# Optimization experiments

Measured on AMD Instinct MI355X. Metric: run time of the kernel, lower is better.

## Reference

```python
import jax, jax.numpy as jnp
import numpy as np

BIAS = 0.0001
TEMPERATURE = 1.0


def setup_inputs() -> dict:
    key = jax.random.key(0)
    k_h, k_w1, k_w2, k_u = jax.random.split(key, 4)
    N, H, Z = 8192, 64, 128
    h = jax.random.normal(k_h, (N, H), dtype=jnp.float32)
    W1 = jax.random.normal(k_w1, (H, H), dtype=jnp.float32) * (1.0 / np.sqrt(H))
    b1 = jnp.zeros((H,), dtype=jnp.float32)
    W2 = jax.random.normal(k_w2, (H, Z), dtype=jnp.float32) * (1.0 / np.sqrt(H))
    b2 = jnp.zeros((Z,), dtype=jnp.float32)
    noise_u = jax.random.uniform(k_u, (N, N), dtype=jnp.float32)
    return {"h": h, "W1": W1, "b1": b1, "W2": W2, "b2": b2, "noise_u": noise_u}


def reference(h, W1, b1, W2, b2, noise_u):
    # MLPA: Linear -> ReLU -> Linear, then outer-product adjacency logits
    Zmat = jnp.maximum(h @ W1 + b1, 0.0) @ W2 + b2          # [N, dim_z]
    adj_logits = Zmat @ Zmat.T                               # [N, N]
    # gumbel-sigmoid edge sampling (training path)
    eps = (2.0 * BIAS - 1.0) * noise_u + (1.0 - BIAS)        # uniform in [bias, 1-bias]
    gate = (jnp.log(eps) - jnp.log1p(-eps) + adj_logits) / TEMPERATURE
    adj = jax.nn.sigmoid(gate)
    # keep strict upper triangle, symmetrize
    adj = jnp.triu(adj, 1)
    adj = adj + adj.T
    # fill_diagonal_(1)
    N = adj.shape[0]
    idx = jnp.arange(N)
    adj = adj.at[idx, idx].set(1.0)
    # D^{-1/2} @ adj @ D^{-1/2} expressed as row/col rescale (same math)
    d = jnp.power(adj.sum(axis=1), -0.5)                     # [N]
    adj_norm = d[:, None] * adj * d[None, :]
    return adj_norm, adj_logits
```

## Files before the change

kernel.cpp:

```cpp
#include <hip/hip_runtime.h>
#include <hip/hip_bf16.h>
#include <math.h>

#define N 8192
#define ZD 128
#define NTILE 64
#define NUPPER 2080

typedef __attribute__((ext_vector_type(8))) _Float16 f16x8;
typedef __attribute__((ext_vector_type(4))) float f32x4;

__device__ __forceinline__ int tri_cum(int ti) {
    return (ti * (2 * NTILE + 1 - ti)) / 2;
}

__device__ __forceinline__ void tile_decode(int t, int& ti, int& tj) {
    int est = (int)((129.0f - sqrtf(16641.0f - 8.0f * (float)t)) * 0.5f);
    if (est < 0) est = 0;
    while (tri_cum(est) > t) --est;
    while (tri_cum(est + 1) <= t) ++est;
    ti = est;
    tj = est + (t - tri_cum(est));
}

__global__ __launch_bounds__(256) void k1_mlp(
    const float* __restrict__ h, const float* __restrict__ W1,
    const float* __restrict__ b1, const float* __restrict__ W2,
    const float* __restrict__ b2, _Float16* __restrict__ Zf,
    float* __restrict__ sums)
{
    __shared__ float W1s[64][65];
    __shared__ float W2s[64][129];
    __shared__ float hs[32][68];
    __shared__ float Ts[32][68];
    __shared__ float b1s[64];
    __shared__ float b2s[128];
    const int tid = threadIdx.x;
    const int row0 = blockIdx.x * 32;

    if (tid < 32) sums[row0 + tid] = 1.0f;

    for (int e = tid; e < 64 * 64; e += 256) W1s[e >> 6][e & 63] = W1[e];
    for (int e = tid; e < 64 * 128; e += 256) W2s[e >> 7][e & 127] = W2[e];
    for (int e = tid; e < 32 * 64; e += 256) hs[e >> 6][e & 63] = h[(size_t)row0 * 64 + e];
    if (tid < 64) b1s[tid] = b1[tid];
    if (tid < 128) b2s[tid] = b2[tid];
    __syncthreads();

    {
        const int c = tid & 63;
        const int r0 = (tid >> 6) * 8;
        float s[8];
        #pragma unroll
        for (int j = 0; j < 8; ++j) s[j] = b1s[c];
        #pragma unroll
        for (int k0 = 0; k0 < 64; k0 += 4) {
            const float w0 = W1s[k0 + 0][c], w1 = W1s[k0 + 1][c];
            const float w2 = W1s[k0 + 2][c], w3 = W1s[k0 + 3][c];
            #pragma unroll
            for (int j = 0; j < 8; ++j) {
                f32x4 hv = *(const f32x4*)&hs[r0 + j][k0];
                s[j] = fmaf(hv[0], w0, s[j]);
                s[j] = fmaf(hv[1], w1, s[j]);
                s[j] = fmaf(hv[2], w2, s[j]);
                s[j] = fmaf(hv[3], w3, s[j]);
            }
        }
        #pragma unroll
        for (int j = 0; j < 8; ++j) Ts[r0 + j][c] = fmaxf(s[j], 0.0f);
    }
    __syncthreads();

    {
        const int c = tid & 127;
        const int r0 = (tid >> 7) * 16;
        float s[16];
        #pragma unroll
        for (int j = 0; j < 16; ++j) s[j] = b2s[c];
        #pragma unroll
        for (int k0 = 0; k0 < 64; k0 += 4) {
            const float w0 = W2s[k0 + 0][c], w1 = W2s[k0 + 1][c];
            const float w2 = W2s[k0 + 2][c], w3 = W2s[k0 + 3][c];
            #pragma unroll
            for (int j = 0; j < 16; ++j) {
                f32x4 tv = *(const f32x4*)&Ts[r0 + j][k0];
                s[j] = fmaf(tv[0], w0, s[j]);
                s[j] = fmaf(tv[1], w1, s[j]);
                s[j] = fmaf(tv[2], w2, s[j]);
                s[j] = fmaf(tv[3], w3, s[j]);
            }
        }
        #pragma unroll
        for (int j = 0; j < 16; ++j)
            Zf[(size_t)(row0 + r0 + j) * ZD + c] = (_Float16)s[j];
    }
}

__global__ __launch_bounds__(256, 3) void k3_main(
    const _Float16* __restrict__ Zf, const float* __restrict__ noise,
    float* __restrict__ logits, unsigned char* __restrict__ vws,
    float* __restrict__ sums)
{
    int ti, tj;
    tile_decode(blockIdx.x, ti, tj);
    const bool diag = (ti == tj);

    __shared__ float T[128][65];
    __shared__ float rs[128], cs[128];

    const int tid = threadIdx.x;
    const int lane = tid & 63;
    const int w = tid >> 6;
    const int wr = w >> 1, wc = w & 1;
    const int fr = lane & 15;
    const int kg = lane >> 4;
    const int i0 = ti * 128, j0 = tj * 128;

    unsigned char* __restrict__ vtile = vws + (size_t)blockIdx.x * (128 * 128);

    if (tid < 128) { rs[tid] = 0.0f; cs[tid] = 0.0f; }

    const _Float16* Ap = Zf + (size_t)(i0 + wr * 64) * ZD;
    const _Float16* Bp = Zf + (size_t)(j0 + wc * 64) * ZD;

    f32x4 acc[4][4];
    #pragma unroll
    for (int mf = 0; mf < 4; ++mf)
        #pragma unroll
        for (int nf = 0; nf < 4; ++nf)
            acc[mf][nf] = (f32x4)0.0f;

    #pragma unroll
    for (int kc = 0; kc < 4; ++kc) {
        const int ko = kc * 32 + kg * 8;
        f16x8 a[4], b[4];
        #pragma unroll
        for (int mf = 0; mf < 4; ++mf) {
            size_t off = (size_t)(mf * 16 + fr) * ZD + ko;
            a[mf] = *(const f16x8*)(Ap + off);
            b[mf] = *(const f16x8*)(Bp + off);
        }
        #pragma unroll
        for (int mf = 0; mf < 4; ++mf)
            #pragma unroll
            for (int nf = 0; nf < 4; ++nf)
                acc[mf][nf] = __builtin_amdgcn_mfma_f32_16x16x32_f16(a[mf], b[nf], acc[mf][nf], 0, 0, 0);
    }

    const int c4 = (tid & 15) * 4;
    const int rbase = tid >> 4;

    #pragma unroll
    for (int half = 0; half < 2; ++half) {
        __syncthreads();
        if (wc == half) {
            #pragma unroll
            for (int mf = 0; mf < 4; ++mf)
                #pragma unroll
                for (int nf = 0; nf < 4; ++nf)
                    #pragma unroll
                    for (int r = 0; r < 4; ++r)
                        T[wr * 64 + mf * 16 + (lane >> 4) * 4 + r][nf * 16 + fr] = acc[mf][nf][r];
        }
        __syncthreads();

        f32x4 csum = (f32x4)0.0f;
        #pragma unroll
        for (int it = 0; it < 8; ++it) {
            const int r = rbase + it * 16;
            f32x4 L4 = *(const f32x4*)&T[r][c4];
            const size_t g = (size_t)(i0 + r) * N + j0 + half * 64 + c4;
            __builtin_nontemporal_store(L4, (f32x4*)&logits[g]);
            f32x4 u4 = __builtin_nontemporal_load((const f32x4*)&noise[g]);
            float rsum = 0.0f;
            unsigned q = 0;
            #pragma unroll
            for (int e = 0; e < 4; ++e) {
                float u = u4[e];
                float eps = fmaf(-0.9998f, u, 0.9999f);
                float om  = fmaf( 0.9998f, u, 0.0001f);
                float gate = __logf(eps) - __logf(om) + L4[e];
                float v = 1.0f / (1.0f + __expf(-gate));
                if (diag && r >= half * 64 + c4 + e) v = 0.0f;
                q |= ((unsigned)(int)rintf(v * 255.0f)) << (8 * e);
                rsum += v;
                csum[e] += v;
            }
            __builtin_nontemporal_store(q, (unsigned*)&vtile[r * 128 + half * 64 + c4]);
            atomicAdd(&rs[r], rsum);
        }
        #pragma unroll
        for (int e = 0; e < 4; ++e)
            atomicAdd(&cs[half * 64 + c4 + e], csum[e]);

        if (!diag) {
            #pragma unroll
            for (int it = 0; it < 8; ++it) {
                const int idx = tid + it * 256;
                const int c = idx >> 5;
                const int m4 = (idx & 31) * 4;
                f32x4 o;
                o[0] = T[m4 + 0][c]; o[1] = T[m4 + 1][c];
                o[2] = T[m4 + 2][c]; o[3] = T[m4 + 3][c];
                __builtin_nontemporal_store(o, (f32x4*)&logits[(size_t)(j0 + half * 64 + c) * N + i0 + m4]);
            }
        }
    }

    __syncthreads();
    if (tid < 128) {
        if (diag) {
            atomicAdd(&sums[i0 + tid], rs[tid] + cs[tid]);
        } else {
            atomicAdd(&sums[i0 + tid], rs[tid]);
            atomicAdd(&sums[j0 + tid], cs[tid]);
        }
    }
}

__global__ __launch_bounds__(256, 4) void k5_norm(
    const unsigned char* __restrict__ vws, float* __restrict__ adj,
    const float* __restrict__ sums)
{
    int ti, tj;
    tile_decode(blockIdx.x, ti, tj);
    const bool diag = (ti == tj);
    __shared__ float T[128][68];
    __shared__ float drow[128], dcol[128];
    const int tid = threadIdx.x;
    const int i0 = ti * 128, j0 = tj * 128;

    const unsigned char* __restrict__ vtile = vws + (size_t)blockIdx.x * (128 * 128);

    if (tid < 128) drow[tid] = rsqrtf(sums[i0 + tid]);
    else dcol[tid - 128] = rsqrtf(sums[j0 + tid - 128]);
    __syncthreads();

    const float inv255 = 1.0f / 255.0f;
    #pragma unroll 4
    for (int it = 0; it < 16; ++it) {
        int w = tid + it * 256;
        int m = w >> 5;
        int n4 = (w & 31) << 2;
        unsigned q = __builtin_nontemporal_load((const unsigned*)&vtile[m * 128 + n4]);
        float dm = drow[m];
        f32x4 o;
        o[0] = (float)(q & 255)         * inv255 * dm * dcol[n4 + 0];
        o[1] = (float)((q >> 8) & 255)  * inv255 * dm * dcol[n4 + 1];
        o[2] = (float)((q >> 16) & 255) * inv255 * dm * dcol[n4 + 2];
        o[3] = (float)(q >> 24)         * inv255 * dm * dcol[n4 + 3];
        __builtin_nontemporal_store(o, (f32x4*)&adj[(size_t)(i0 + m) * N + j0 + n4]);
        T[n4 + 0][m] = o[0]; T[n4 + 1][m] = o[1];
        T[n4 + 2][m] = o[2]; T[n4 + 3][m] = o[3];
    }
    __syncthreads();
    #pragma unroll 4
    for (int it = 0; it < 16; ++it) {
        int w = tid + it * 256;
        int c = w >> 5;
        int m4 = (w & 31) << 2;
        f32x4 o = *(const f32x4*)&T[c][m4];
        if (!diag) {
            __builtin_nontemporal_store(o, (f32x4*)&adj[(size_t)(j0 + c) * N + i0 + m4]);
        } else {
            #pragma unroll
            for (int e = 0; e < 4; ++e)
                if (m4 + e < c)
                    adj[(size_t)(j0 + c) * N + i0 + m4 + e] = o[e];
        }
    }
    if (diag && tid < 128) {
        float dm = drow[tid];
        adj[(size_t)(i0 + tid) * N + i0 + tid] = dm * dm;
    }
}

extern "C" void kernel_launch(void* const* d_in, const int* in_sizes, int n_in,
                              void* d_out, int out_size, void* d_ws, size_t ws_size,
                              hipStream_t stream)
{
    const float* h     = (const float*)d_in[0];
    const float* W1    = (const float*)d_in[1];
    const float* b1    = (const float*)d_in[2];
    const float* W2    = (const float*)d_in[3];
    const float* b2    = (const float*)d_in[4];
    const float* noise = (const float*)d_in[5];

    float* adj    = (float*)d_out;
    float* logits = adj + (size_t)N * N;

    _Float16* Zf       = (_Float16*)d_ws;
    unsigned char* vws = (unsigned char*)(Zf + (size_t)N * ZD);
    float* sums        = (float*)(vws + (size_t)NUPPER * 128 * 128);

    k1_mlp<<<256, 256, 0, stream>>>(h, W1, b1, W2, b2, Zf, sums);
    k3_main<<<NUPPER, 256, 0, stream>>>(Zf, noise, logits, vws, sums);
    k5_norm<<<NUPPER, 256, 0, stream>>>(vws, adj, sums);
}
```

Measured before the change: 230.2 us.

## Write full symmetric quantized adjacency in main kernel and stream rows in norm pass

```diff
diff --git a/kernel.cpp b/kernel.cpp
--- a/kernel.cpp
+++ b/kernel.cpp
@@ -9,6 +9,7 @@
 
 typedef __attribute__((ext_vector_type(8))) _Float16 f16x8;
 typedef __attribute__((ext_vector_type(4))) float f32x4;
+typedef __attribute__((ext_vector_type(4))) unsigned int u32x4;
 
 __device__ __forceinline__ int tri_cum(int ti) {
     return (ti * (2 * NTILE + 1 - ti)) / 2;
@@ -70,7 +71,6 @@
         for (int j = 0; j < 8; ++j) Ts[r0 + j][c] = fmaxf(s[j], 0.0f);
     }
     __syncthreads();
-
     {
         const int c = tid & 127;
         const int r0 = (tid >> 7) * 16;
@@ -96,17 +96,24 @@
     }
 }
 
-__global__ __launch_bounds__(256, 3) void k3_main(
+#define AROW 136
+
+__global__ __launch_bounds__(256, 2) void k3_main(
     const _Float16* __restrict__ Zf, const float* __restrict__ noise,
-    float* __restrict__ logits, unsigned char* __restrict__ vws,
+    float* __restrict__ logits, unsigned char* __restrict__ vfull,
     float* __restrict__ sums)
 {
     int ti, tj;
-    tile_decode(blockIdx.x, ti, tj);
+    const int t = (blockIdx.x & 7) * (NUPPER / 8) + (blockIdx.x >> 3);
+    tile_decode(t, ti, tj);
     const bool diag = (ti == tj);
 
-    __shared__ float T[128][65];
+    __shared__ _Float16 smem[2 * 128 * AROW];
     __shared__ float rs[128], cs[128];
+    _Float16* As = smem;
+    _Float16* Bs = smem + 128 * AROW;
+    float (*T)[65] = (float(*)[65])smem;
+    unsigned char* vT = (unsigned char*)(smem + 128 * AROW);
 
     const int tid = threadIdx.x;
     const int lane = tid & 63;
@@ -116,12 +123,15 @@
     const int kg = lane >> 4;
     const int i0 = ti * 128, j0 = tj * 128;
 
-    unsigned char* __restrict__ vtile = vws + (size_t)blockIdx.x * (128 * 128);
-
+    #pragma unroll
+    for (int p = 0; p < 8; ++p) {
+        const int c = tid + p * 256;
+        const int row = c >> 4, cg = (c & 15) << 3;
+        *(f16x8*)&As[row * AROW + cg] = *(const f16x8*)(Zf + (size_t)(i0 + row) * ZD + cg);
+        *(f16x8*)&Bs[row * AROW + cg] = *(const f16x8*)(Zf + (size_t)(j0 + row) * ZD + cg);
+    }
     if (tid < 128) { rs[tid] = 0.0f; cs[tid] = 0.0f; }
-
-    const _Float16* Ap = Zf + (size_t)(i0 + wr * 64) * ZD;
-    const _Float16* Bp = Zf + (size_t)(j0 + wc * 64) * ZD;
+    __syncthreads();
 
     f32x4 acc[4][4];
     #pragma unroll
@@ -136,9 +146,8 @@
         f16x8 a[4], b[4];
         #pragma unroll
         for (int mf = 0; mf < 4; ++mf) {
-            size_t off = (size_t)(mf * 16 + fr) * ZD + ko;
-            a[mf] = *(const f16x8*)(Ap + off);
-            b[mf] = *(const f16x8*)(Bp + off);
+            a[mf] = *(const f16x8*)&As[(wr * 64 + mf * 16 + fr) * AROW + ko];
+            b[mf] = *(const f16x8*)&Bs[(wc * 64 + mf * 16 + fr) * AROW + ko];
         }
         #pragma unroll
         for (int mf = 0; mf < 4; ++mf)
@@ -169,7 +178,8 @@
         for (int it = 0; it < 8; ++it) {
             const int r = rbase + it * 16;
             f32x4 L4 = *(const f32x4*)&T[r][c4];
-            const size_t g = (size_t)(i0 + r) * N + j0 + half * 64 + c4;
+            const int lc0 = half * 64 + c4;
+            const size_t g = (size_t)(i0 + r) * N + j0 + lc0;
             __builtin_nontemporal_store(L4, (f32x4*)&logits[g]);
             f32x4 u4 = __builtin_nontemporal_load((const f32x4*)&noise[g]);
             float rsum = 0.0f;
@@ -181,28 +191,47 @@
                 float om  = fmaf( 0.9998f, u, 0.0001f);
                 float gate = __logf(eps) - __logf(om) + L4[e];
                 float v = 1.0f / (1.0f + __expf(-gate));
-                if (diag && r >= half * 64 + c4 + e) v = 0.0f;
+                if (diag && r >= lc0 + e) v = 0.0f;
                 q |= ((unsigned)(int)rintf(v * 255.0f)) << (8 * e);
                 rsum += v;
                 csum[e] += v;
             }
-            __builtin_nontemporal_store(q, (unsigned*)&vtile[r * 128 + half * 64 + c4]);
+            if (!diag) {
+                __builtin_nontemporal_store(q, (unsigned*)&vfull[g]);
+            } else {
+                #pragma unroll
+                for (int e = 0; e < 4; ++e)
+                    if (r < lc0 + e) vfull[g + e] = (unsigned char)((q >> (8 * e)) & 255);
+            }
+            #pragma unroll
+            for (int e = 0; e < 4; ++e)
+                vT[(c4 + e) * 128 + r] = (unsigned char)((q >> (8 * e)) & 255);
             atomicAdd(&rs[r], rsum);
         }
         #pragma unroll
         for (int e = 0; e < 4; ++e)
             atomicAdd(&cs[half * 64 + c4 + e], csum[e]);
 
-        if (!diag) {
-            #pragma unroll
-            for (int it = 0; it < 8; ++it) {
-                const int idx = tid + it * 256;
-                const int c = idx >> 5;
-                const int m4 = (idx & 31) * 4;
+        __syncthreads();
+
+        #pragma unroll
+        for (int it = 0; it < 8; ++it) {
+            const int idx = tid + it * 256;
+            const int c = idx >> 5;
+            const int m4 = (idx & 31) * 4;
+            const unsigned qd = *(const unsigned*)&vT[c * 128 + m4];
+            if (!diag) {
                 f32x4 o;
                 o[0] = T[m4 + 0][c]; o[1] = T[m4 + 1][c];
                 o[2] = T[m4 + 2][c]; o[3] = T[m4 + 3][c];
                 __builtin_nontemporal_store(o, (f32x4*)&logits[(size_t)(j0 + half * 64 + c) * N + i0 + m4]);
+                __builtin_nontemporal_store(qd, (unsigned*)&vfull[(size_t)(j0 + half * 64 + c) * N + i0 + m4]);
+            } else {
+                const int rr = half * 64 + c;
+                #pragma unroll
+                for (int e = 0; e < 4; ++e)
+                    if (m4 + e < rr)
+                        vfull[(size_t)(i0 + rr) * N + i0 + m4 + e] = (unsigned char)((qd >> (8 * e)) & 255);
             }
         }
     }
@@ -218,60 +247,51 @@
     }
 }
 
-__global__ __launch_bounds__(256, 4) void k5_norm(
-    const unsigned char* __restrict__ vws, float* __restrict__ adj,
-    const float* __restrict__ sums)
-{
-    int ti, tj;
-    tile_decode(blockIdx.x, ti, tj);
-    const bool diag = (ti == tj);
-    __shared__ float T[128][68];
-    __shared__ float drow[128], dcol[128];
+__global__ void k4_dvec(const float* __restrict__ sums, float* __restrict__ dvec)
+{
+    int i = blockIdx.x * 256 + threadIdx.x;
+    if (i < N) dvec[i] = rsqrtf(sums[i]);
+}
+
+__global__ __launch_bounds__(256) void k5_norm(
+    const unsigned char* __restrict__ vfull, float* __restrict__ adj,
+    const float* __restrict__ dvec)
+{
+    __shared__ float dc[N];
     const int tid = threadIdx.x;
-    const int i0 = ti * 128, j0 = tj * 128;
-
-    const unsigned char* __restrict__ vtile = vws + (size_t)blockIdx.x * (128 * 128);
-
-    if (tid < 128) drow[tid] = rsqrtf(sums[i0 + tid]);
-    else dcol[tid - 128] = rsqrtf(sums[j0 + tid - 128]);
-    __syncthreads();
-
-    const float inv255 = 1.0f / 255.0f;
-    #pragma unroll 4
+    #pragma unroll
+    for (int p = 0; p < 8; ++p) {
+        const int e = (tid + p * 256) * 4;
+        *(f32x4*)&dc[e] = *(const f32x4*)&dvec[e];
+    }
+    __syncthreads();
+
+    const int row = blockIdx.x * 8 + (tid >> 5);
+    const float di = dc[row];
+    const float sdi = di * (1.0f / 255.0f);
+    const size_t rowbase = (size_t)row * N;
+    const int lane32 = tid & 31;
+
     for (int it = 0; it < 16; ++it) {
-        int w = tid + it * 256;
-        int m = w >> 5;
-        int n4 = (w & 31) << 2;
-        unsigned q = __builtin_nontemporal_load((const unsigned*)&vtile[m * 128 + n4]);
-        float dm = drow[m];
-        f32x4 o;
-        o[0] = (float)(q & 255)         * inv255 * dm * dcol[n4 + 0];
-        o[1] = (float)((q >> 8) & 255)  * inv255 * dm * dcol[n4 + 1];
-        o[2] = (float)((q >> 16) & 255) * inv255 * dm * dcol[n4 + 2];
-        o[3] = (float)(q >> 24)         * inv255 * dm * dcol[n4 + 3];
-        __builtin_nontemporal_store(o, (f32x4*)&adj[(size_t)(i0 + m) * N + j0 + n4]);
-        T[n4 + 0][m] = o[0]; T[n4 + 1][m] = o[1];
-        T[n4 + 2][m] = o[2]; T[n4 + 3][m] = o[3];
-    }
-    __syncthreads();
-    #pragma unroll 4
-    for (int it = 0; it < 16; ++it) {
-        int w = tid + it * 256;
-        int c = w >> 5;
-        int m4 = (w & 31) << 2;
-        f32x4 o = *(const f32x4*)&T[c][m4];
-        if (!diag) {
-            __builtin_nontemporal_store(o, (f32x4*)&adj[(size_t)(j0 + c) * N + i0 + m4]);
-        } else {
-            #pragma unroll
-            for (int e = 0; e < 4; ++e)
-                if (m4 + e < c)
-                    adj[(size_t)(j0 + c) * N + i0 + m4 + e] = o[e];
-        }
-    }
-    if (diag && tid < 128) {
-        float dm = drow[tid];
-        adj[(size_t)(i0 + tid) * N + i0 + tid] = dm * dm;
+        const int j = (lane32 + it * 32) * 16;
+        u32x4 qv = __builtin_nontemporal_load((const u32x4*)&vfull[rowbase + j]);
+        const bool hasdiag = ((unsigned)(row - j) < 16u);
+        #pragma unroll
+        for (int k = 0; k < 4; ++k) {
+            f32x4 dk = *(const f32x4*)&dc[j + 4 * k];
+            const unsigned qd = qv[k];
+            f32x4 o;
+            o[0] = (float)(qd & 255)         * sdi * dk[0];
+            o[1] = (float)((qd >> 8) & 255)  * sdi * dk[1];
+            o[2] = (float)((qd >> 16) & 255) * sdi * dk[2];
+            o[3] = (float)(qd >> 24)         * sdi * dk[3];
+            if (hasdiag) {
+                #pragma unroll
+                for (int e = 0; e < 4; ++e)
+                    if (j + 4 * k + e == row) o[e] = di * di;
+            }
+            __builtin_nontemporal_store(o, (f32x4*)&adj[rowbase + j + 4 * k]);
+        }
     }
 }
 
@@ -289,11 +309,13 @@
     float* adj    = (float*)d_out;
     float* logits = adj + (size_t)N * N;
 
-    _Float16* Zf       = (_Float16*)d_ws;
-    unsigned char* vws = (unsigned char*)(Zf + (size_t)N * ZD);
-    float* sums        = (float*)(vws + (size_t)NUPPER * 128 * 128);
+    _Float16* Zf         = (_Float16*)d_ws;
+    unsigned char* vfull = (unsigned char*)(Zf + (size_t)N * ZD);
+    float* sums          = (float*)(vfull + (size_t)N * N);
+    float* dvec          = sums + N;
 
     k1_mlp<<<256, 256, 0, stream>>>(h, W1, b1, W2, b2, Zf, sums);
-    k3_main<<<NUPPER, 256, 0, stream>>>(Zf, noise, logits, vws, sums);
-    k5_norm<<<NUPPER, 256, 0, stream>>>(vws, adj, sums);
-}
+    k3_main<<<NUPPER, 256, 0, stream>>>(Zf, noise, logits, vfull, sums);
+    k4_dvec<<<32, 256, 0, stream>>>(sums, dvec);
+    k5_norm<<<N / 8, 256, 0, stream>>>(vfull, adj, dvec);
+}
```

Measured after the change: 686.1 us. 2.98x slower.

## Split k3 tiles into half-width blocks and write results directly from MFMA registers

Applied to the files above, without the earlier changes.

```diff
diff --git a/kernel.cpp b/kernel.cpp
--- a/kernel.cpp
+++ b/kernel.cpp
@@ -70,7 +70,6 @@
         for (int j = 0; j < 8; ++j) Ts[r0 + j][c] = fmaxf(s[j], 0.0f);
     }
     __syncthreads();
-
     {
         const int c = tid & 127;
         const int r0 = (tid >> 7) * 16;
@@ -96,126 +95,114 @@
     }
 }
 
-__global__ __launch_bounds__(256, 3) void k3_main(
+__global__ __launch_bounds__(256, 5) void k3_main(
     const _Float16* __restrict__ Zf, const float* __restrict__ noise,
     float* __restrict__ logits, unsigned char* __restrict__ vws,
     float* __restrict__ sums)
 {
+    const int tt = blockIdx.x >> 1;
+    const int t = (tt & 7) * (NUPPER / 8) + (tt >> 3);
+    const int h = blockIdx.x & 1;
     int ti, tj;
-    tile_decode(blockIdx.x, ti, tj);
+    tile_decode(t, ti, tj);
     const bool diag = (ti == tj);
-
-    __shared__ float T[128][65];
-    __shared__ float rs[128], cs[128];
+    const int i0 = ti * 128;
+    const int j0 = tj * 128 + h * 64;
+
+    __shared__ unsigned char vTT[128 * 68];
+    __shared__ float rs[128], cs[64];
 
     const int tid = threadIdx.x;
     const int lane = tid & 63;
     const int w = tid >> 6;
-    const int wr = w >> 1, wc = w & 1;
+    const int wr = w >> 1, wcc = w & 1;
     const int fr = lane & 15;
     const int kg = lane >> 4;
-    const int i0 = ti * 128, j0 = tj * 128;
-
-    unsigned char* __restrict__ vtile = vws + (size_t)blockIdx.x * (128 * 128);
-
-    if (tid < 128) { rs[tid] = 0.0f; cs[tid] = 0.0f; }
+
+    if (tid < 128) rs[tid] = 0.0f;
+    if (tid < 64) cs[tid] = 0.0f;
 
     const _Float16* Ap = Zf + (size_t)(i0 + wr * 64) * ZD;
-    const _Float16* Bp = Zf + (size_t)(j0 + wc * 64) * ZD;
-
-    f32x4 acc[4][4];
+    const _Float16* Bp = Zf + (size_t)(j0 + wcc * 32) * ZD;
+
+    f32x4 acc[4][2];
     #pragma unroll
     for (int mf = 0; mf < 4; ++mf)
         #pragma unroll
-        for (int nf = 0; nf < 4; ++nf)
+        for (int nf = 0; nf < 2; ++nf)
             acc[mf][nf] = (f32x4)0.0f;
 
     #pragma unroll
     for (int kc = 0; kc < 4; ++kc) {
         const int ko = kc * 32 + kg * 8;
-        f16x8 a[4], b[4];
-        #pragma unroll
-        for (int mf = 0; mf < 4; ++mf) {
-            size_t off = (size_t)(mf * 16 + fr) * ZD + ko;
-            a[mf] = *(const f16x8*)(Ap + off);
-            b[mf] = *(const f16x8*)(Bp + off);
-        }
+        f16x8 a[4], b[2];
         #pragma unroll
         for (int mf = 0; mf < 4; ++mf)
-            #pragma unroll
-            for (int nf = 0; nf < 4; ++nf)
+            a[mf] = *(const f16x8*)(Ap + (size_t)(mf * 16 + fr) * ZD + ko);
+        #pragma unroll
+        for (int nf = 0; nf < 2; ++nf)
+            b[nf] = *(const f16x8*)(Bp + (size_t)(nf * 16 + fr) * ZD + ko);
+        #pragma unroll
+        for (int mf = 0; mf < 4; ++mf)
+            #pragma unroll
+            for (int nf = 0; nf < 2; ++nf)
                 acc[mf][nf] = __builtin_amdgcn_mfma_f32_16x16x32_f16(a[mf], b[nf], acc[mf][nf], 0, 0, 0);
     }
-
-    const int c4 = (tid & 15) * 4;
-    const int rbase = tid >> 4;
-
-    #pragma unroll
-    for (int half = 0; half < 2; ++half) {
-        __syncthreads();
-        if (wc == half) {
-            #pragma unroll
-            for (int mf = 0; mf < 4; ++mf)
-                #pragma unroll
-                for (int nf = 0; nf < 4; ++nf)
-                    #pragma unroll
-                    for (int r = 0; r < 4; ++r)
-                        T[wr * 64 + mf * 16 + (lane >> 4) * 4 + r][nf * 16 + fr] = acc[mf][nf][r];
-        }
-        __syncthreads();
-
-        f32x4 csum = (f32x4)0.0f;
-        #pragma unroll
-        for (int it = 0; it < 8; ++it) {
-            const int r = rbase + it * 16;
-            f32x4 L4 = *(const f32x4*)&T[r][c4];
-            const size_t g = (size_t)(i0 + r) * N + j0 + half * 64 + c4;
-            __builtin_nontemporal_store(L4, (f32x4*)&logits[g]);
-            f32x4 u4 = __builtin_nontemporal_load((const f32x4*)&noise[g]);
-            float rsum = 0.0f;
+    __syncthreads();
+
+    float cacc[2] = {0.f, 0.f};
+    #pragma unroll
+    for (int mf = 0; mf < 4; ++mf) {
+        const int Rl = wr * 64 + mf * 16 + (lane >> 4) * 4;
+        f32x4 rsum4 = (f32x4)0.0f;
+        #pragma unroll
+        for (int nf = 0; nf < 2; ++nf) {
+            const int Cl = wcc * 32 + nf * 16 + (lane & 15);
+            const f32x4 Lv = acc[mf][nf];
+            const size_t gi = (size_t)(i0 + Rl) * N + (j0 + Cl);
+            #pragma unroll
+            for (int k = 0; k < 4; ++k)
+                __builtin_nontemporal_store(Lv[k], &logits[gi + (size_t)k * N]);
+            __builtin_nontemporal_store(Lv, (f32x4*)&logits[(size_t)(j0 + Cl) * N + (i0 + Rl)]);
             unsigned q = 0;
             #pragma unroll
-            for (int e = 0; e < 4; ++e) {
-                float u = u4[e];
+            for (int k = 0; k < 4; ++k) {
+                float u = __builtin_nontemporal_load(&noise[gi + (size_t)k * N]);
                 float eps = fmaf(-0.9998f, u, 0.9999f);
                 float om  = fmaf( 0.9998f, u, 0.0001f);
-                float gate = __logf(eps) - __logf(om) + L4[e];
+                float gate = __logf(eps) - __logf(om) + Lv[k];
                 float v = 1.0f / (1.0f + __expf(-gate));
-                if (diag && r >= half * 64 + c4 + e) v = 0.0f;
-                q |= ((unsigned)(int)rintf(v * 255.0f)) << (8 * e);
-                rsum += v;
-                csum[e] += v;
+                if (diag && (i0 + Rl + k) >= (j0 + Cl)) v = 0.0f;
+                q |= ((unsigned)(int)rintf(v * 255.0f)) << (8 * k);
+                rsum4[k] += v;
+                cacc[nf] += v;
             }
-            __builtin_nontemporal_store(q, (unsigned*)&vtile[r * 128 + half * 64 + c4]);
-            atomicAdd(&rs[r], rsum);
-        }
-        #pragma unroll
-        for (int e = 0; e < 4; ++e)
-            atomicAdd(&cs[half * 64 + c4 + e], csum[e]);
-
-        if (!diag) {
-            #pragma unroll
-            for (int it = 0; it < 8; ++it) {
-                const int idx = tid + it * 256;
-                const int c = idx >> 5;
-                const int m4 = (idx & 31) * 4;
-                f32x4 o;
-                o[0] = T[m4 + 0][c]; o[1] = T[m4 + 1][c];
-                o[2] = T[m4 + 2][c]; o[3] = T[m4 + 3][c];
-                __builtin_nontemporal_store(o, (f32x4*)&logits[(size_t)(j0 + half * 64 + c) * N + i0 + m4]);
-            }
-        }
-    }
-
-    __syncthreads();
-    if (tid < 128) {
-        if (diag) {
-            atomicAdd(&sums[i0 + tid], rs[tid] + cs[tid]);
-        } else {
-            atomicAdd(&sums[i0 + tid], rs[tid]);
-            atomicAdd(&sums[j0 + tid], cs[tid]);
-        }
-    }
+            #pragma unroll
+            for (int k = 0; k < 4; ++k)
+                vTT[(Rl + k) * 68 + Cl] = (unsigned char)((q >> (8 * k)) & 255);
+        }
+        #pragma unroll
+        for (int k = 0; k < 4; ++k)
+            atomicAdd(&rs[Rl + k], rsum4[k]);
+    }
+    #pragma unroll
+    for (int nf = 0; nf < 2; ++nf)
+        atomicAdd(&cs[wcc * 32 + nf * 16 + (lane & 15)], cacc[nf]);
+
+    __syncthreads();
+
+    unsigned char* __restrict__ vtile = vws + (size_t)t * (128 * 128);
+    #pragma unroll
+    for (int it = 0; it < 8; ++it) {
+        const int idx = tid + it * 256;
+        const int r = idx >> 4;
+        const int c4 = (idx & 15) * 4;
+        const unsigned q = *(const unsigned*)&vTT[r * 68 + c4];
+        __builtin_nontemporal_store(q, (unsigned*)&vtile[r * 128 + h * 64 + c4]);
+    }
+
+    if (tid < 128) atomicAdd(&sums[i0 + tid], rs[tid]);
+    if (tid < 64)  atomicAdd(&sums[j0 + tid], cs[tid]);
 }
 
 __global__ __launch_bounds__(256, 4) void k5_norm(
@@ -294,6 +281,6 @@
     float* sums        = (float*)(vws + (size_t)NUPPER * 128 * 128);
 
     k1_mlp<<<256, 256, 0, stream>>>(h, W1, b1, W2, b2, Zf, sums);
-    k3_main<<<NUPPER, 256, 0, stream>>>(Zf, noise, logits, vws, sums);
+    k3_main<<<NUPPER * 2, 256, 0, stream>>>(Zf, noise, logits, vws, sums);
     k5_norm<<<NUPPER, 256, 0, stream>>>(vws, adj, sums);
 }
```

Result: slower. 275.1 us (+19.5%).
